# Kernel tuning notes

Hardware: AMD Instinct MI355X
Metric: run time of the kernel (lower is better)

## Reference

```python
import jax, jax.numpy as jnp
import numpy as np

N, C, H, W = 16, 256, 128, 128
TC = max(8, C // 32)  # temp_c
EPS = 1e-5


def setup_inputs() -> dict:
    key = jax.random.key(0)
    ks = jax.random.split(key, 10)
    x = jax.random.normal(ks[0], (N, C, H, W), jnp.float32)
    # conv1: 1x1, C -> TC (weight squeezed to [TC, C])
    w1 = jax.random.normal(ks[1], (TC, C), jnp.float32) * 0.05
    b1 = jnp.zeros((TC,), jnp.float32)
    # BatchNorm2d (inference form)
    bn_gamma = jnp.ones((TC,), jnp.float32)
    bn_beta = jnp.zeros((TC,), jnp.float32)
    bn_mean = jnp.zeros((TC,), jnp.float32)
    bn_var = jnp.ones((TC,), jnp.float32)
    # conv2: kernel (1,2), TC -> C, squeezed to [C, TC, 2]
    w2 = jax.random.normal(ks[2], (C, TC, 2), jnp.float32) * 0.1
    b2 = jnp.zeros((C,), jnp.float32)
    # conv3: kernel (2,1), TC -> C, squeezed to [C, TC, 2]
    w3 = jax.random.normal(ks[3], (C, TC, 2), jnp.float32) * 0.1
    b3 = jnp.zeros((C,), jnp.float32)
    # conv4: kernel (1,2), TC -> C, squeezed to [C, TC, 2]
    w4 = jax.random.normal(ks[4], (C, TC, 2), jnp.float32) * 0.1
    b4 = jnp.zeros((C,), jnp.float32)
    return dict(x=x, w1=w1, b1=b1, bn_gamma=bn_gamma, bn_beta=bn_beta,
                bn_mean=bn_mean, bn_var=bn_var, w2=w2, b2=b2, w3=w3, b3=b3,
                w4=w4, b4=b4)


def reference(x, w1, b1, bn_gamma, bn_beta, bn_mean, bn_var,
              w2, b2, w3, b3, w4, b4):
    n, c, Hh, Ww = x.shape
    # avg/max pools along W (per-row), H (per-col), and global (per-channel)
    cat_h = jnp.stack([x.mean(3), x.max(3)], axis=-1)            # [n,c,H,2]
    cat_w = jnp.stack([x.mean(2), x.max(2)], axis=-1)            # [n,c,W,2]
    cat_c = jnp.stack([x.mean((2, 3)), x.max((2, 3))], -1)[:, :, None, :]  # [n,c,1,2]
    x_cat = jnp.concatenate([cat_h, cat_w, cat_c], axis=2)       # [n,c,H+W+1,2]
    # 1x1 conv + BN (inference) + h_swish
    y = jnp.einsum('ncsk,tc->ntsk', x_cat, w1) + b1[None, :, None, None]
    inv = bn_gamma / jnp.sqrt(bn_var + EPS)
    y = (y - bn_mean[None, :, None, None]) * inv[None, :, None, None] \
        + bn_beta[None, :, None, None]
    y = y * jnp.clip(y + 3.0, 0.0, 6.0) / 6.0                    # h_swish
    # split
    xh = y[:, :, :Hh, :]               # [n,tc,H,2]
    xw = y[:, :, Hh:Hh + Ww, :]        # [n,tc,W,2]
    xc = y[:, :, Hh + Ww, :]           # [n,tc,2]
    # tiny convs (kernels collapse to contractions over (tc, k)) + sigmoid
    a_h = jax.nn.sigmoid(jnp.einsum('nthk,otk->noh', xh, w2) + b2[None, :, None])  # [n,C,H]
    a_w = jax.nn.sigmoid(jnp.einsum('ntwk,otk->now', xw, w3) + b3[None, :, None])  # [n,C,W]
    a_c = jax.nn.sigmoid(jnp.einsum('ntk,otk->no', xc, w4) + b4[None, :])          # [n,C]
    return x * a_w[:, :, None, :] * a_h[:, :, :, None] * a_c[:, :, None, None]
```

## Files before the change

kernel.cpp:

```cpp
#include <hip/hip_runtime.h>
#include <math.h>

#define N_ 16
#define C_ 256
#define H_ 128
#define W_ 128
#define TC_ 8
#define S_ 257
#define EPS_ 1e-5f
#define NBLK 512
#define BPN 32
#define PPB 8

#define XCT_OFF  0
#define AH_OFF   2105344
#define AW_OFF   (AH_OFF + 524288)
#define Y256_OFF (AW_OFF + 524288)

typedef float f4n __attribute__((ext_vector_type(4)));

template <int CTRL>
__device__ __forceinline__ float dpp_zf(float x) {
    return __int_as_float(__builtin_amdgcn_update_dpp(
        0, __float_as_int(x), CTRL, 0xF, 0xF, true));
}
template <int CTRL>
__device__ __forceinline__ float dpp_keep(float x) {
    return __int_as_float(__builtin_amdgcn_update_dpp(
        __float_as_int(x), __float_as_int(x), CTRL, 0xF, 0xF, false));
}
#define SHR1 0x111
#define SHR2 0x112
#define SHR4 0x114
#define SHR8 0x118
#define BC15 0x142

__device__ __forceinline__ float rowsum32(float x) {
    x += dpp_zf<SHR1>(x);
    x += dpp_zf<SHR2>(x);
    x += dpp_zf<SHR4>(x);
    x += dpp_zf<SHR8>(x);
    x += dpp_zf<BC15>(x);
    return x;
}
__device__ __forceinline__ float rowmax32(float x) {
    x = fmaxf(x, dpp_keep<SHR1>(x));
    x = fmaxf(x, dpp_keep<SHR2>(x));
    x = fmaxf(x, dpp_keep<SHR4>(x));
    x = fmaxf(x, dpp_keep<SHR8>(x));
    x = fmaxf(x, dpp_keep<BC15>(x));
    return x;
}

__global__ __launch_bounds__(256, 4) void k1_stats(
    const float* __restrict__ x, float* __restrict__ xcat)
{
    const int tid = threadIdx.x, lane = tid & 63, wv = tid >> 6;
    const int p = blockIdx.x * 4 + wv;
    const float4* xt = reinterpret_cast<const float4*>(x) + (size_t)p * 4096;
    float2* xcat2 = reinterpret_cast<float2*>(xcat) + (size_t)p * S_;

    float4 cs = make_float4(0.f, 0.f, 0.f, 0.f);
    float4 cm = make_float4(-INFINITY, -INFINITY, -INFINITY, -INFINITY);

    #pragma unroll 8
    for (int it = 0; it < 64; ++it) {
        const float4 v = xt[it * 64 + lane];
        cs.x += v.x; cs.y += v.y; cs.z += v.z; cs.w += v.w;
        cm.x = fmaxf(cm.x, v.x); cm.y = fmaxf(cm.y, v.y);
        cm.z = fmaxf(cm.z, v.z); cm.w = fmaxf(cm.w, v.w);

        float rs = (v.x + v.y) + (v.z + v.w);
        float rm = fmaxf(fmaxf(v.x, v.y), fmaxf(v.z, v.w));
        rs = rowsum32(rs);
        rm = rowmax32(rm);
        if ((lane & 31) == 31)
            xcat2[it * 2 + (lane >> 5)] = make_float2(rs * (1.f / 128.f), rm);
    }

    cs.x += __shfl_xor(cs.x, 32); cs.y += __shfl_xor(cs.y, 32);
    cs.z += __shfl_xor(cs.z, 32); cs.w += __shfl_xor(cs.w, 32);
    cm.x = fmaxf(cm.x, __shfl_xor(cm.x, 32));
    cm.y = fmaxf(cm.y, __shfl_xor(cm.y, 32));
    cm.z = fmaxf(cm.z, __shfl_xor(cm.z, 32));
    cm.w = fmaxf(cm.w, __shfl_xor(cm.w, 32));

    if (lane < 32) {
        const int w0 = 4 * lane;
        xcat2[128 + w0 + 0] = make_float2(cs.x * (1.f / 128.f), cm.x);
        xcat2[128 + w0 + 1] = make_float2(cs.y * (1.f / 128.f), cm.y);
        xcat2[128 + w0 + 2] = make_float2(cs.z * (1.f / 128.f), cm.z);
        xcat2[128 + w0 + 3] = make_float2(cs.w * (1.f / 128.f), cm.w);
    }

    float gs = (cs.x + cs.y) + (cs.z + cs.w);
    float gm = fmaxf(fmaxf(cm.x, cm.y), fmaxf(cm.z, cm.w));
    #pragma unroll
    for (int m = 16; m >= 1; m >>= 1) {
        gs += __shfl_xor(gs, m);
        gm = fmaxf(gm, __shfl_xor(gm, m));
    }
    if (lane == 0) xcat2[256] = make_float2(gs * (1.f / 16384.f), gm);
}

__global__ __launch_bounds__(256, 2) void k2_attn(
    const float* __restrict__ xcat,
    const float* __restrict__ w1, const float* __restrict__ b1,
    const float* __restrict__ gam, const float* __restrict__ bet,
    const float* __restrict__ mu, const float* __restrict__ var,
    const float* __restrict__ w2, const float* __restrict__ b2,
    const float* __restrict__ w3, const float* __restrict__ b3,
    float* __restrict__ ahg, float* __restrict__ awg, float* __restrict__ y256g)
{
    const int b = blockIdx.x;
    const int n = b >> 5, cg = b & 31;
    const int tid = threadIdx.x;
    __shared__ __align__(16) float smf[6448];

    float* w1s = smf;
    float* red = smf + 2048;
    float* ys  = smf + 6272;
    const float2* xc2 = reinterpret_cast<const float2*>(xcat) + (size_t)n * C_ * S_;
    const int s0 = cg * 8;

    for (int i = tid; i < TC_ * C_; i += 256) w1s[i] = w1[i];
    __syncthreads();

    {
        const int cgrp = tid >> 3, si = tid & 7;
        const int s = s0 + si;
        float acc[16];
        #pragma unroll
        for (int j = 0; j < 16; ++j) acc[j] = 0.f;
        #pragma unroll
        for (int i = 0; i < 8; ++i) {
            const int c = cgrp * 8 + i;
            const float2 v = xc2[c * S_ + s];
            #pragma unroll
            for (int t = 0; t < TC_; ++t) {
                const float w = w1s[t * C_ + c];
                acc[t * 2 + 0] += v.x * w;
                acc[t * 2 + 1] += v.y * w;
            }
        }
        #pragma unroll
        for (int j = 0; j < 16; ++j) red[(si * 16 + j) * 33 + cgrp] = acc[j];
    }
    __syncthreads();

    if (tid < 128) {
        const int si2 = tid >> 4, j = tid & 15, t = j >> 1;
        float z = 0.f;
        #pragma unroll
        for (int g = 0; g < 32; ++g) z += red[(si2 * 16 + j) * 33 + g];
        const float inv = gam[t] * rsqrtf(var[t] + EPS_);
        float y = (z + b1[t] - mu[t]) * inv + bet[t];
        y = y * fminf(fmaxf(y + 3.f, 0.f), 6.f) * (1.f / 6.f);
        ys[si2 * 17 + j] = y;
    }
    __syncthreads();

    if (cg == BPN - 1) {
        const int c = tid;
        const float2 v = xc2[c * S_ + 256];
        float pj[16];
        #pragma unroll
        for (int t = 0; t < TC_; ++t) {
            const float w = w1s[t * C_ + c];
            pj[t * 2 + 0] = v.x * w;
            pj[t * 2 + 1] = v.y * w;
        }
        __syncthreads();
        float* red2 = smf;
        float* redB = smf + 4400;
        #pragma unroll
        for (int j = 0; j < 16; ++j) red2[tid * 17 + j] = pj[j];
        __syncthreads();
        {
            const int g = tid >> 4, j = tid & 15;
            float z = 0.f;
            #pragma unroll
            for (int m = 0; m < 16; ++m) z += red2[(g * 16 + m) * 17 + j];
            redB[j * 17 + g] = z;
        }
        __syncthreads();
        if (tid < 16) {
            const int j = tid, t = j >> 1;
            float z = 0.f;
            #pragma unroll
            for (int g = 0; g < 16; ++g) z += redB[j * 17 + g];
            const float inv = gam[t] * rsqrtf(var[t] + EPS_);
            float y = (z + b1[t] - mu[t]) * inv + bet[t];
            y = y * fminf(fmaxf(y + 3.f, 0.f), 6.f) * (1.f / 6.f);
            y256g[n * 16 + j] = y;
        }
        __syncthreads();
    }

    {
        const int o = tid;
        const bool is_h = (cg < 16);
        const float* wX = is_h ? w2 : w3;
        const float zb = is_h ? b2[o] : b3[o];
        float4 wr[4];
        const float4* wv = reinterpret_cast<const float4*>(wX + o * 16);
        #pragma unroll
        for (int q = 0; q < 4; ++q) wr[q] = wv[q];

        float r[8];
        #pragma unroll
        for (int si = 0; si < 8; ++si) {
            float z = zb;
            #pragma unroll
            for (int q = 0; q < 4; ++q) {
                z += ys[si * 17 + q * 4 + 0] * wr[q].x
                   + ys[si * 17 + q * 4 + 1] * wr[q].y
                   + ys[si * 17 + q * 4 + 2] * wr[q].z
                   + ys[si * 17 + q * 4 + 3] * wr[q].w;
            }
            r[si] = 1.f / (1.f + expf(-z));
        }
        float* og = is_h ? (ahg + (size_t)(n * C_ + o) * H_ + s0)
                         : (awg + (size_t)(n * C_ + o) * W_ + (s0 - 128));
        *reinterpret_cast<float4*>(og)     = make_float4(r[0], r[1], r[2], r[3]);
        *reinterpret_cast<float4*>(og + 4) = make_float4(r[4], r[5], r[6], r[7]);
    }
}

__global__ __launch_bounds__(256, 2) void k3_apply(
    const float* __restrict__ x,
    const float* __restrict__ w4, const float* __restrict__ b4,
    const float* __restrict__ ahg, const float* __restrict__ awg,
    const float* __restrict__ y256g, float* __restrict__ out)
{
    const int b = blockIdx.x;
    const int n = b >> 5, cg = b & 31, c0 = cg * 8;
    const int tid = threadIdx.x;
    __shared__ __align__(16) float smf[2064];

    float* acs = smf;
    float* ahl = smf + 16;
    float* awl = smf + 1040;

    if (tid < 8) {
        const int o = c0 + tid;
        float z = b4[o];
        #pragma unroll
        for (int j = 0; j < 16; ++j) z += y256g[n * 16 + j] * w4[o * 16 + j];
        acs[tid] = 1.f / (1.f + expf(-z));
    }
    __syncthreads();

    for (int idx = tid; idx < 8 * 128; idx += 256) {
        const int u = idx >> 7, h = idx & 127, o = c0 + u;
        ahl[idx] = acs[u] * ahg[(size_t)(n * C_ + o) * H_ + h];
        awl[idx] = awg[(size_t)(n * C_ + o) * W_ + h];
    }
    __syncthreads();

    const float4* awv = reinterpret_cast<const float4*>(awl);
    for (int u = 0; u < PPB; ++u) {
        const int p = b * PPB + u;
        const f4n* x4 = reinterpret_cast<const f4n*>(x) + (size_t)p * 4096;
        f4n* o4 = reinterpret_cast<f4n*>(out) + (size_t)p * 4096;

        const float4 a = awv[u * 32 + (tid & 31)];
        #pragma unroll
        for (int k = 0; k < 16; ++k) {
            const int i4 = k * 256 + tid;
            f4n v = x4[i4];
            const float s = ahl[u * 128 + k * 8 + (tid >> 5)];
            v.x *= s * a.x; v.y *= s * a.y; v.z *= s * a.z; v.w *= s * a.w;
            o4[i4] = v;
        }
    }
}

extern "C" void kernel_launch(void* const* d_in, const int* in_sizes, int n_in,
                              void* d_out, int out_size, void* d_ws, size_t ws_size,
                              hipStream_t stream) {
    const float* x   = (const float*)d_in[0];
    const float* w1  = (const float*)d_in[1];
    const float* b1  = (const float*)d_in[2];
    const float* gam = (const float*)d_in[3];
    const float* bet = (const float*)d_in[4];
    const float* mu  = (const float*)d_in[5];
    const float* var = (const float*)d_in[6];
    const float* w2  = (const float*)d_in[7];
    const float* b2  = (const float*)d_in[8];
    const float* w3  = (const float*)d_in[9];
    const float* b3  = (const float*)d_in[10];
    const float* w4  = (const float*)d_in[11];
    const float* b4  = (const float*)d_in[12];

    float* ws    = (float*)d_ws;
    float* xcat  = ws + XCT_OFF;
    float* ahg   = ws + AH_OFF;
    float* awg   = ws + AW_OFF;
    float* y256g = ws + Y256_OFF;
    float* out   = (float*)d_out;

    k1_stats<<<1024, 256, 0, stream>>>(x, xcat);
    k2_attn<<<NBLK, 256, 0, stream>>>(xcat, w1, b1, gam, bet, mu, var,
                                      w2, b2, w3, b3, ahg, awg, y256g);
    k3_apply<<<NBLK, 256, 0, stream>>>(x, w4, b4, ahg, awg, y256g, out);
}
```

Measured before the change: 186.5 us.

## Restructure apply kernel to one wave per plane with nontemporal stores

The apply kernel now maps each 64-lane wavefront to a single (n,c) plane and launches 1024 blocks of four waves instead of 512 blocks each processing eight planes. The shared-memory staging and both block barriers are removed; each wave computes its own channel gate and reads the row/column gates directly from global memory. Output stores use nontemporal hints to avoid polluting cache, and launch bounds allow more resident blocks. The intent is more parallelism and less synchronization in this bandwidth-bound pass, at the cost of redundant gate loads per wave.

```diff
diff --git a/kernel.cpp b/kernel.cpp
--- a/kernel.cpp
+++ b/kernel.cpp
@@ -10,7 +10,6 @@
 #define EPS_ 1e-5f
 #define NBLK 512
 #define BPN 32
-#define PPB 8
 
 #define XCT_OFF  0
 #define AH_OFF   2105344
@@ -227,52 +226,39 @@
     }
 }
 
-__global__ __launch_bounds__(256, 2) void k3_apply(
+__global__ __launch_bounds__(256, 4) void k3_apply(
     const float* __restrict__ x,
     const float* __restrict__ w4, const float* __restrict__ b4,
     const float* __restrict__ ahg, const float* __restrict__ awg,
     const float* __restrict__ y256g, float* __restrict__ out)
 {
-    const int b = blockIdx.x;
-    const int n = b >> 5, cg = b & 31, c0 = cg * 8;
-    const int tid = threadIdx.x;
-    __shared__ __align__(16) float smf[2064];
-
-    float* acs = smf;
-    float* ahl = smf + 16;
-    float* awl = smf + 1040;
-
-    if (tid < 8) {
-        const int o = c0 + tid;
-        float z = b4[o];
-        #pragma unroll
-        for (int j = 0; j < 16; ++j) z += y256g[n * 16 + j] * w4[o * 16 + j];
-        acs[tid] = 1.f / (1.f + expf(-z));
-    }
-    __syncthreads();
-
-    for (int idx = tid; idx < 8 * 128; idx += 256) {
-        const int u = idx >> 7, h = idx & 127, o = c0 + u;
-        ahl[idx] = acs[u] * ahg[(size_t)(n * C_ + o) * H_ + h];
-        awl[idx] = awg[(size_t)(n * C_ + o) * W_ + h];
-    }
-    __syncthreads();
-
-    const float4* awv = reinterpret_cast<const float4*>(awl);
-    for (int u = 0; u < PPB; ++u) {
-        const int p = b * PPB + u;
-        const f4n* x4 = reinterpret_cast<const f4n*>(x) + (size_t)p * 4096;
-        f4n* o4 = reinterpret_cast<f4n*>(out) + (size_t)p * 4096;
-
-        const float4 a = awv[u * 32 + (tid & 31)];
-        #pragma unroll
-        for (int k = 0; k < 16; ++k) {
-            const int i4 = k * 256 + tid;
-            f4n v = x4[i4];
-            const float s = ahl[u * 128 + k * 8 + (tid >> 5)];
-            v.x *= s * a.x; v.y *= s * a.y; v.z *= s * a.z; v.w *= s * a.w;
-            o4[i4] = v;
-        }
+    const int tid = threadIdx.x, lane = tid & 63, wv = tid >> 6;
+    const int p = blockIdx.x * 4 + wv;
+    const int n = p >> 8, o = p & 255;
+
+    float z = b4[o];
+    const float4* w4v = reinterpret_cast<const float4*>(w4 + o * 16);
+    const float4* yv  = reinterpret_cast<const float4*>(y256g + n * 16);
+    #pragma unroll
+    for (int q = 0; q < 4; ++q) {
+        const float4 ww = w4v[q], yy = yv[q];
+        z += yy.x * ww.x + yy.y * ww.y + yy.z * ww.z + yy.w * ww.w;
+    }
+    const float ac = 1.f / (1.f + expf(-z));
+
+    const float4 aw = reinterpret_cast<const float4*>(awg + (size_t)p * W_)[lane & 31];
+
+    const f4n* x4 = reinterpret_cast<const f4n*>(x) + (size_t)p * 4096;
+    f4n* o4 = reinterpret_cast<f4n*>(out) + (size_t)p * 4096;
+    const float* ah = ahg + (size_t)p * H_;
+    const int half = lane >> 5;
+
+    #pragma unroll 8
+    for (int it = 0; it < 64; ++it) {
+        f4n v = x4[it * 64 + lane];
+        const float s = ac * ah[2 * it + half];
+        v.x *= s * aw.x; v.y *= s * aw.y; v.z *= s * aw.z; v.w *= s * aw.w;
+        __builtin_nontemporal_store(v, &o4[it * 64 + lane]);
     }
 }
 
@@ -303,5 +289,5 @@
     k1_stats<<<1024, 256, 0, stream>>>(x, xcat);
     k2_attn<<<NBLK, 256, 0, stream>>>(xcat, w1, b1, gam, bet, mu, var,
                                       w2, b2, w3, b3, ahg, awg, y256g);
-    k3_apply<<<NBLK, 256, 0, stream>>>(x, w4, b4, ahg, awg, y256g, out);
-}
+    k3_apply<<<1024, 256, 0, stream>>>(x, w4, b4, ahg, awg, y256g, out);
+}
```

After: 155.2 us. -16.8%, faster.
